# Kernel tuning notes

Hardware: AMD Instinct MI355X
Metric: run time of the kernel (lower is better)

## Reference

```python
import jax, jax.numpy as jnp
import numpy as np

HEADS = 4  # from init_kwargs

def _branch_index(seq_len: int) -> jnp.ndarray:
    # position 0 -> layer_s(0), 1 -> layer_r(1), 2 -> layer_o(2),
    # then alternating layer_a(3)/layer_v(4) starting at position 3.
    tail = jnp.where((jnp.arange(seq_len - 3) % 2) == 0, 3, 4)
    return jnp.concatenate([jnp.array([0, 1, 2], dtype=tail.dtype), tail])


def setup_inputs() -> dict:
    key = jax.random.key(0)
    k1, k2, k3 = jax.random.split(key, 3)
    B, S, H = 128, 513, 256
    x = jax.random.normal(k1, (B, S, H), dtype=jnp.float32)
    # 5 Linear layers, nn.Linear convention: y = x @ W.T + b, W: [out,in]
    W = jax.random.normal(k2, (5, H, H), dtype=jnp.float32) * (1.0 / np.sqrt(H))
    b = jax.random.normal(k3, (5, H), dtype=jnp.float32) * 0.02
    return {"x": x, "W": W, "b": b}


def reference(x, W, b):
    # Original applies each Linear to a position-masked copy of x and sums.
    # Since the 5 masks are disjoint one-hots over positions, the weight term
    # at position t is x[t] @ W[m(t)].T; the bias term is sum of ALL 5 biases
    # (Linear(0) = bias), applied at every position.
    B, S, H = x.shape
    idx = _branch_index(S)            # [S] in {0..4}
    Wsel = W[idx]
    out = jnp.einsum('bsh,sdh->bsd', x, Wsel) + b.sum(axis=0)
    return out.reshape(B, S, HEADS, H // HEADS)
```

## Files before the change

kernel.cpp:

```cpp
#include <hip/hip_runtime.h>
#include <hip/hip_bf16.h>

#define B_ 128
#define S_ 513
#define H_ 256

typedef __attribute__((ext_vector_type(8))) short short8;
typedef __attribute__((ext_vector_type(4))) float f32x4;

static __device__ inline unsigned short f2bf(float f) {
    union { float f; unsigned int u; } v; v.f = f;
    unsigned int u = v.u;
    unsigned int r = u + 0x7fffu + ((u >> 16) & 1u);
    return (unsigned short)(r >> 16);
}

__global__ __launch_bounds__(256, 3)
void sel_gemm_kernel(const float* __restrict__ x,
                     const float* __restrict__ W,
                     const float* __restrict__ bias,
                     float* __restrict__ out) {
    const int bx = blockIdx.x;
    const int s  = bx >> 1;
    const int h  = bx & 1;
    const int m_idx = (s < 3) ? s : ((s & 1) ? 3 : 4);

    __shared__ unsigned short As[64 * 72];
    __shared__ unsigned short Bs[256 * 72];

    const int t    = threadIdx.x;
    const int lane = t & 63;
    const int w    = t >> 6;
    const int lrow = lane & 15;
    const int quad = lane >> 4;

    const float* xbase = x + ((size_t)(h * 64) * S_ + s) * H_;
    const float* Wbase = W + (size_t)m_idx * H_ * H_;

    f32x4 acc[4][4];
#pragma unroll
    for (int i = 0; i < 4; ++i)
#pragma unroll
        for (int j = 0; j < 4; ++j) {
            f32x4 z = {0.f, 0.f, 0.f, 0.f};
            acc[i][j] = z;
        }

    for (int kt = 0; kt < 4; ++kt) {
        const int k0 = kt * 64;
        __syncthreads();

#pragma unroll
        for (int i = 0; i < 4; ++i) {
            int flat = i * 256 + t;
            int row  = flat >> 4;
            int col  = (flat & 15) * 4;
            const float4 v = *(const float4*)(xbase + (size_t)row * (S_ * H_) + k0 + col);
            ushort4 p;
            p.x = f2bf(v.x); p.y = f2bf(v.y); p.z = f2bf(v.z); p.w = f2bf(v.w);
            *(ushort4*)&As[row * 72 + col] = p;
        }
#pragma unroll 8
        for (int i = 0; i < 16; ++i) {
            int flat = i * 256 + t;
            int row  = flat >> 4;
            int col  = (flat & 15) * 4;
            const float4 v = *(const float4*)(Wbase + (size_t)row * H_ + k0 + col);
            ushort4 p;
            p.x = f2bf(v.x); p.y = f2bf(v.y); p.z = f2bf(v.z); p.w = f2bf(v.w);
            *(ushort4*)&Bs[row * 72 + col] = p;
        }
        __syncthreads();

#pragma unroll
        for (int kk = 0; kk < 64; kk += 32) {
            const int kf = kk + quad * 8;
            short8 a_frag[4], b_frag[4];
#pragma unroll
            for (int i = 0; i < 4; ++i)
                a_frag[i] = *(const short8*)&As[(i * 16 + lrow) * 72 + kf];
#pragma unroll
            for (int j = 0; j < 4; ++j)
                b_frag[j] = *(const short8*)&Bs[(w * 64 + j * 16 + lrow) * 72 + kf];
#pragma unroll
            for (int i = 0; i < 4; ++i)
#pragma unroll
                for (int j = 0; j < 4; ++j)
                    acc[i][j] = __builtin_amdgcn_mfma_f32_16x16x32_bf16(
                        a_frag[i], b_frag[j], acc[i][j], 0, 0, 0);
        }
    }

    float bsum[4];
#pragma unroll
    for (int j = 0; j < 4; ++j) {
        int d = w * 64 + j * 16 + lrow;
        float sum = 0.f;
#pragma unroll
        for (int i = 0; i < 5; ++i) sum += bias[i * H_ + d];
        bsum[j] = sum;
    }

#pragma unroll
    for (int i = 0; i < 4; ++i) {
#pragma unroll
        for (int r = 0; r < 4; ++r) {
            int bg = h * 64 + i * 16 + quad * 4 + r;
            float* orow = out + ((size_t)bg * S_ + s) * H_;
#pragma unroll
            for (int j = 0; j < 4; ++j) {
                int d = w * 64 + j * 16 + lrow;
                orow[d] = acc[i][j][r] + bsum[j];
            }
        }
    }
}

extern "C" void kernel_launch(void* const* d_in, const int* in_sizes, int n_in,
                              void* d_out, int out_size, void* d_ws, size_t ws_size,
                              hipStream_t stream) {
    const float* x    = (const float*)d_in[0];
    const float* W    = (const float*)d_in[1];
    const float* bias = (const float*)d_in[2];
    float* out = (float*)d_out;

    dim3 grid(S_ * 2);
    dim3 block(256);
    sel_gemm_kernel<<<grid, block, 0, stream>>>(x, W, bias, out);
}
```

Measured before the change: 140.4 us.

## Stage full x tile in LDS once and load W fragments directly from global

Loads the entire 64x256 activation tile into shared memory up front and drops the shared-memory staging of W. Each wave instead reads its own W rows straight from global (L2) into registers and converts them to bf16 in-register, which removes the per-k-tile barriers and the LDS footprint for W. The tradeoff is less coalesced, latency-exposed global loads of W inside the MFMA loop.

Result: slower. 154.5 us (+10.0%).

```diff
diff --git a/kernel.cpp b/kernel.cpp
--- a/kernel.cpp
+++ b/kernel.cpp
@@ -7,6 +7,15 @@
 
 typedef __attribute__((ext_vector_type(8))) short short8;
 typedef __attribute__((ext_vector_type(4))) float f32x4;
+
+static __device__ inline short8 pack8(float4 a, float4 b) {
+    union { short8 s; __hip_bfloat162 h[4]; } u;
+    u.h[0] = __float22bfloat162_rn(make_float2(a.x, a.y));
+    u.h[1] = __float22bfloat162_rn(make_float2(a.z, a.w));
+    u.h[2] = __float22bfloat162_rn(make_float2(b.x, b.y));
+    u.h[3] = __float22bfloat162_rn(make_float2(b.z, b.w));
+    return u.s;
+}
 
 static __device__ inline unsigned short f2bf(float f) {
     union { float f; unsigned int u; } v; v.f = f;
@@ -25,8 +34,7 @@
     const int h  = bx & 1;
     const int m_idx = (s < 3) ? s : ((s & 1) ? 3 : 4);
 
-    __shared__ unsigned short As[64 * 72];
-    __shared__ unsigned short Bs[256 * 72];
+    __shared__ unsigned short As[64 * 264];
 
     const int t    = threadIdx.x;
     const int lane = t & 63;
@@ -37,6 +45,17 @@
     const float* xbase = x + ((size_t)(h * 64) * S_ + s) * H_;
     const float* Wbase = W + (size_t)m_idx * H_ * H_;
 
+#pragma unroll
+    for (int i = 0; i < 16; ++i) {
+        int flat = i * 256 + t;
+        int row  = flat >> 6;
+        int col  = (flat & 63) * 4;
+        const float4 v = *(const float4*)(xbase + (size_t)row * (S_ * H_) + col);
+        ushort4 p;
+        p.x = f2bf(v.x); p.y = f2bf(v.y); p.z = f2bf(v.z); p.w = f2bf(v.w);
+        *(ushort4*)&As[row * 264 + col] = p;
+    }
+
     f32x4 acc[4][4];
 #pragma unroll
     for (int i = 0; i < 4; ++i)
@@ -46,48 +65,29 @@
             acc[i][j] = z;
         }
 
-    for (int kt = 0; kt < 4; ++kt) {
-        const int k0 = kt * 64;
-        __syncthreads();
+    const float* Wrow[4];
+#pragma unroll
+    for (int j = 0; j < 4; ++j)
+        Wrow[j] = Wbase + (size_t)(w * 64 + j * 16 + lrow) * H_;
 
+    __syncthreads();
+
+#pragma unroll 2
+    for (int kk = 0; kk < 8; ++kk) {
+        const int kf = kk * 32 + quad * 8;
+        short8 a_frag[4];
 #pragma unroll
-        for (int i = 0; i < 4; ++i) {
-            int flat = i * 256 + t;
-            int row  = flat >> 4;
-            int col  = (flat & 15) * 4;
-            const float4 v = *(const float4*)(xbase + (size_t)row * (S_ * H_) + k0 + col);
-            ushort4 p;
-            p.x = f2bf(v.x); p.y = f2bf(v.y); p.z = f2bf(v.z); p.w = f2bf(v.w);
-            *(ushort4*)&As[row * 72 + col] = p;
-        }
-#pragma unroll 8
-        for (int i = 0; i < 16; ++i) {
-            int flat = i * 256 + t;
-            int row  = flat >> 4;
-            int col  = (flat & 15) * 4;
-            const float4 v = *(const float4*)(Wbase + (size_t)row * H_ + k0 + col);
-            ushort4 p;
-            p.x = f2bf(v.x); p.y = f2bf(v.y); p.z = f2bf(v.z); p.w = f2bf(v.w);
-            *(ushort4*)&Bs[row * 72 + col] = p;
-        }
-        __syncthreads();
-
+        for (int i = 0; i < 4; ++i)
+            a_frag[i] = *(const short8*)&As[(i * 16 + lrow) * 264 + kf];
 #pragma unroll
-        for (int kk = 0; kk < 64; kk += 32) {
-            const int kf = kk + quad * 8;
-            short8 a_frag[4], b_frag[4];
+        for (int j = 0; j < 4; ++j) {
+            const float4 w0 = *(const float4*)(Wrow[j] + kf);
+            const float4 w1 = *(const float4*)(Wrow[j] + kf + 4);
+            const short8 b_frag = pack8(w0, w1);
 #pragma unroll
             for (int i = 0; i < 4; ++i)
-                a_frag[i] = *(const short8*)&As[(i * 16 + lrow) * 72 + kf];
-#pragma unroll
-            for (int j = 0; j < 4; ++j)
-                b_frag[j] = *(const short8*)&Bs[(w * 64 + j * 16 + lrow) * 72 + kf];
-#pragma unroll
-            for (int i = 0; i < 4; ++i)
-#pragma unroll
-                for (int j = 0; j < 4; ++j)
-                    acc[i][j] = __builtin_amdgcn_mfma_f32_16x16x32_bf16(
-                        a_frag[i], b_frag[j], acc[i][j], 0, 0, 0);
+                acc[i][j] = __builtin_amdgcn_mfma_f32_16x16x32_bf16(
+                    a_frag[i], b_frag, acc[i][j], 0, 0, 0);
         }
     }
 
```
